# Kernel optimization log

Measured on AMD Instinct MI355X. Metric: run time of the kernel, lower is better.

Reference implementation:

```python
import jax, jax.numpy as jnp
import numpy as np

B, S, D = 2, 512, 256

def setup_inputs() -> dict:
    key = jax.random.key(0)
    k1, k2, k3, k4, k5 = jax.random.split(key, 5)
    return {
        "query": jax.random.normal(k1, (B, S, D), dtype=jnp.float32),
        "key": jax.random.normal(k2, (B, S, D), dtype=jnp.float32),
        "value": jax.random.normal(k3, (B, S, D), dtype=jnp.float32),
        "Wm_w": jax.random.normal(k4, (D, D), dtype=jnp.float32) * (1.0 / np.sqrt(D)),
        "vm_w": jax.random.normal(k5, (1, D), dtype=jnp.float32) * (1.0 / np.sqrt(D)),
    }

def reference(query, key, value, Wm_w, vm_w):
    # pairwise difference: q.unsqueeze(1) - q.unsqueeze(2) -> [B, S, S, D]
    diff = query[:, None, :, :] - query[:, :, None, :]
    # Wm (Linear, no bias): [B,S,S,D] @ Wm_w^T, then tanh
    h = jnp.tanh(jnp.einsum('bijd,ed->bije', diff, Wm_w))
    # vm (Linear D->1, no bias) + squeeze -> scores [B, S, S]
    sjt = jnp.einsum('bije,e->bij', h, vm_w[0])
    # softmax over dim=2 (eval mode: dropout is identity)
    atten = jax.nn.softmax(sjt, axis=2)
    # bmm(atten, value) -> [B, S, D]
    context = jnp.einsum('bij,bjd->bid', atten, value)
    return context, atten
```

## Files before the change

### kernel.cpp

```cpp
#include <hip/hip_runtime.h>

#define B 2
#define S 512
#define D 256
#define C2L 2.885390081777927f
#define LOG2E 1.4426950408889634f

typedef float f32x2 __attribute__((ext_vector_type(2)));
typedef unsigned int u32x2 __attribute__((ext_vector_type(2)));

__global__ __launch_bounds__(256) void proj_kernel(const float* __restrict__ q,
                                                   const float* __restrict__ W,
                                                   float* __restrict__ EJ4,
                                                   float* __restrict__ EN) {
    __shared__ float qlds[4 * D];
    const int t = threadIdx.x;
    const int b = blockIdx.x / (S / 4);
    const int i0 = (blockIdx.x % (S / 4)) * 4;
    const float* qbase = q + (size_t)(b * S + i0) * D;
    for (int idx = t; idx < 4 * D; idx += 256) qlds[idx] = qbase[idx];
    __syncthreads();
    const float* wr = W + (size_t)t * D;
    float a0 = 0.f, a1 = 0.f, a2 = 0.f, a3 = 0.f;
#pragma unroll 4
    for (int d = 0; d < D; ++d) {
        float w = wr[d];
        a0 = fmaf(qlds[d], w, a0);
        a1 = fmaf(qlds[D + d], w, a1);
        a2 = fmaf(qlds[2 * D + d], w, a2);
        a3 = fmaf(qlds[3 * D + d], w, a3);
    }
    a0 *= C2L; a1 *= C2L; a2 *= C2L; a3 *= C2L;
    float* ejb = EJ4 + (((size_t)(b * 64 + (t >> 2))) * S + i0) * 4 + (t & 3);
    ejb[0]  = __builtin_amdgcn_exp2f(a0);
    ejb[4]  = __builtin_amdgcn_exp2f(a1);
    ejb[8]  = __builtin_amdgcn_exp2f(a2);
    ejb[12] = __builtin_amdgcn_exp2f(a3);
    EN[(size_t)(b * S + i0 + 0) * D + t] = __builtin_amdgcn_exp2f(-a0);
    EN[(size_t)(b * S + i0 + 1) * D + t] = __builtin_amdgcn_exp2f(-a1);
    EN[(size_t)(b * S + i0 + 2) * D + t] = __builtin_amdgcn_exp2f(-a2);
    EN[(size_t)(b * S + i0 + 3) * D + t] = __builtin_amdgcn_exp2f(-a3);
}

__global__ __launch_bounds__(512) void fused_kernel(const float* __restrict__ EJ4,
                                                    const float* __restrict__ EN,
                                                    const float* __restrict__ vm,
                                                    const float* __restrict__ value,
                                                    float* __restrict__ att,
                                                    float* __restrict__ ctx) {
    __shared__ float en4[D][4];
    __shared__ float wl[D];
    __shared__ float a4[S][4];
    __shared__ float part[4][8][64][4];
    __shared__ float redm[4][8], reds[4][8];

    const int t = threadIdx.x;
    const int b = blockIdx.x >> 7;
    const int i0 = (blockIdx.x & 127) * 4;

    if (t < D) wl[t] = -2.f * vm[t];
    {
        const int e = t & 255, rsel = t >> 8;
        float v0 = EN[((size_t)(b * S + i0 + rsel)) * D + e];
        float v2 = EN[((size_t)(b * S + i0 + rsel + 2)) * D + e];
        en4[e][rsel * 2 + 0] = v0;
        en4[e][rsel * 2 + 1] = v2;
    }
    __syncthreads();

    f32x2 acc02 = {0.f, 0.f}, acc13 = {0.f, 0.f};
    const float4* ejp = (const float4*)EJ4 + (size_t)b * 64 * S + t;
    const f32x2 one2 = {1.f, 1.f}, two2 = {2.f, 2.f};
    const u32x2 magic = {0x7EF311C3u, 0x7EF311C3u};
#pragma unroll 4
    for (int g = 0; g < 64; ++g) {
        float4 ev4 = ejp[(size_t)g * S];
#pragma unroll
        for (int c = 0; c < 4; ++c) {
            const float ev = (c == 0) ? ev4.x : (c == 1) ? ev4.y : (c == 2) ? ev4.z : ev4.w;
            const int e = g * 4 + c;
            float4 f = *(const float4*)&en4[e][0];
            const float w = wl[e];
            f32x2 ev2 = {ev, ev};
            f32x2 f02 = {f.x, f.y}, f13 = {f.z, f.w};
            f32x2 y02 = ev2 * f02 + one2;
            f32x2 y13 = ev2 * f13 + one2;
            f32x2 r02 = {__builtin_amdgcn_rcpf(y02.x),
                         __builtin_amdgcn_rcpf(y02.y)};
            u32x2 ui = magic - __builtin_bit_cast(u32x2, y13);
            f32x2 rn = __builtin_bit_cast(f32x2, ui);
            rn = rn * (two2 - y13 * rn);
            rn = rn * (two2 - y13 * rn);
            f32x2 w2 = {w, w};
            acc02 += w2 * r02;
            acc13 += w2 * rn;
        }
    }
    float accR[4] = {acc02.x, acc13.x, acc02.y, acc13.y};

    const int lane = t & 63, wv = t >> 6;
#pragma unroll
    for (int r = 0; r < 4; ++r) {
        float lm = accR[r];
#pragma unroll
        for (int off = 32; off; off >>= 1) lm = fmaxf(lm, __shfl_xor(lm, off));
        if (lane == 0) redm[r][wv] = lm;
    }
    __syncthreads();
    float p[4];
#pragma unroll
    for (int r = 0; r < 4; ++r) {
        float m = redm[r][0];
#pragma unroll
        for (int w = 1; w < 8; ++w) m = fmaxf(m, redm[r][w]);
        p[r] = __builtin_amdgcn_exp2f((accR[r] - m) * LOG2E);
        float ls = p[r];
#pragma unroll
        for (int off = 32; off; off >>= 1) ls += __shfl_xor(ls, off);
        if (lane == 0) reds[r][wv] = ls;
    }
    __syncthreads();
#pragma unroll
    for (int r = 0; r < 4; ++r) {
        float s = 0.f;
#pragma unroll
        for (int w = 0; w < 8; ++w) s += reds[r][w];
        float a = p[r] * __builtin_amdgcn_rcpf(s);
        a4[t][r] = a;
        att[(size_t)(b * S + i0 + r) * S + t] = a;
    }
    __syncthreads();

    {
        const int dq = t & 63, js = t >> 6;
        float4 acc0 = {}, acc1 = {}, acc2 = {}, acc3 = {};
        const float* vb = value + (size_t)b * S * D + (size_t)dq * 4;
#pragma unroll 4
        for (int jj = 0; jj < 64; ++jj) {
            int j = js * 64 + jj;
            float4 v = *(const float4*)(vb + (size_t)j * D);
            float w0 = a4[j][0], w1 = a4[j][1], w2 = a4[j][2], w3 = a4[j][3];
            acc0.x = fmaf(w0, v.x, acc0.x); acc0.y = fmaf(w0, v.y, acc0.y);
            acc0.z = fmaf(w0, v.z, acc0.z); acc0.w = fmaf(w0, v.w, acc0.w);
            acc1.x = fmaf(w1, v.x, acc1.x); acc1.y = fmaf(w1, v.y, acc1.y);
            acc1.z = fmaf(w1, v.z, acc1.z); acc1.w = fmaf(w1, v.w, acc1.w);
            acc2.x = fmaf(w2, v.x, acc2.x); acc2.y = fmaf(w2, v.y, acc2.y);
            acc2.z = fmaf(w2, v.z, acc2.z); acc2.w = fmaf(w2, v.w, acc2.w);
            acc3.x = fmaf(w3, v.x, acc3.x); acc3.y = fmaf(w3, v.y, acc3.y);
            acc3.z = fmaf(w3, v.z, acc3.z); acc3.w = fmaf(w3, v.w, acc3.w);
        }
        *(float4*)&part[0][js][dq][0] = acc0;
        *(float4*)&part[1][js][dq][0] = acc1;
        *(float4*)&part[2][js][dq][0] = acc2;
        *(float4*)&part[3][js][dq][0] = acc3;
    }
    __syncthreads();
    if (t < 256) {
        const int row = t >> 6, dq = t & 63;
        float4 sum = {};
#pragma unroll
        for (int js = 0; js < 8; ++js) {
            float4 pt = *(const float4*)&part[row][js][dq][0];
            sum.x += pt.x; sum.y += pt.y; sum.z += pt.z; sum.w += pt.w;
        }
        *(float4*)(ctx + (size_t)(b * S + i0 + row) * D + (size_t)dq * 4) = sum;
    }
}

extern "C" void kernel_launch(void* const* d_in, const int* in_sizes, int n_in,
                              void* d_out, int out_size, void* d_ws, size_t ws_size,
                              hipStream_t stream) {
    const float* q = (const float*)d_in[0];
    const float* value = (const float*)d_in[2];
    const float* W = (const float*)d_in[3];
    const float* vm = (const float*)d_in[4];

    float* ctx = (float*)d_out;
    float* att = ctx + (size_t)B * S * D;
    float* EJ4 = (float*)d_ws;
    float* EN = EJ4 + (size_t)B * D * S;

    proj_kernel<<<B * (S / 4), 256, 0, stream>>>(q, W, EJ4, EN);
    fused_kernel<<<B * (S / 4), 512, 0, stream>>>(EJ4, EN, vm, value, att, ctx);
}
```

Before: 44.57 us.

## Split score reduction over E across two thread halves in fused kernel

Doubles the fused kernel's block size to 1024 threads and splits the 256-wide E reduction of the score computation into two halves of 128. Each half writes its partial sums to a new shared buffer, and the first 512 threads combine them before the softmax and context stages. The aim is more latency hiding and more waves for the transcendental-heavy score loop on a grid of only 256 blocks. The cost is extra shared memory, an additional barrier, and half the threads sitting idle during softmax and the value matmul.

```diff
diff --git a/kernel.cpp b/kernel.cpp
--- a/kernel.cpp
+++ b/kernel.cpp
@@ -42,14 +42,15 @@
     EN[(size_t)(b * S + i0 + 3) * D + t] = __builtin_amdgcn_exp2f(-a3);
 }
 
-__global__ __launch_bounds__(512) void fused_kernel(const float* __restrict__ EJ4,
-                                                    const float* __restrict__ EN,
-                                                    const float* __restrict__ vm,
-                                                    const float* __restrict__ value,
-                                                    float* __restrict__ att,
-                                                    float* __restrict__ ctx) {
+__global__ __launch_bounds__(1024) void fused_kernel(const float* __restrict__ EJ4,
+                                                     const float* __restrict__ EN,
+                                                     const float* __restrict__ vm,
+                                                     const float* __restrict__ value,
+                                                     float* __restrict__ att,
+                                                     float* __restrict__ ctx) {
     __shared__ float en4[D][4];
     __shared__ float wl[D];
+    __shared__ float4 comb[2][S];
     __shared__ float a4[S][4];
     __shared__ float part[4][8][64][4];
     __shared__ float redm[4][8], reds[4][8];
@@ -58,27 +59,26 @@
     const int b = blockIdx.x >> 7;
     const int i0 = (blockIdx.x & 127) * 4;
 
-    if (t < D) wl[t] = -2.f * vm[t];
     {
-        const int e = t & 255, rsel = t >> 8;
-        float v0 = EN[((size_t)(b * S + i0 + rsel)) * D + e];
-        float v2 = EN[((size_t)(b * S + i0 + rsel + 2)) * D + e];
-        en4[e][rsel * 2 + 0] = v0;
-        en4[e][rsel * 2 + 1] = v2;
+        const int e = t & 255, r = t >> 8;
+        const int comp = ((r & 1) << 1) | (r >> 1);
+        en4[e][comp] = EN[((size_t)(b * S + i0 + r)) * D + e];
+        if (r == 0) wl[e] = -2.f * vm[e];
     }
     __syncthreads();
 
+    const int j = t & 511, eh = t >> 9;
     f32x2 acc02 = {0.f, 0.f}, acc13 = {0.f, 0.f};
-    const float4* ejp = (const float4*)EJ4 + (size_t)b * 64 * S + t;
+    const float4* ejp = (const float4*)EJ4 + ((size_t)(b * 64 + eh * 32)) * S + j;
     const f32x2 one2 = {1.f, 1.f}, two2 = {2.f, 2.f};
     const u32x2 magic = {0x7EF311C3u, 0x7EF311C3u};
-#pragma unroll 4
-    for (int g = 0; g < 64; ++g) {
+#pragma unroll 8
+    for (int g = 0; g < 32; ++g) {
         float4 ev4 = ejp[(size_t)g * S];
 #pragma unroll
         for (int c = 0; c < 4; ++c) {
             const float ev = (c == 0) ? ev4.x : (c == 1) ? ev4.y : (c == 2) ? ev4.z : ev4.w;
-            const int e = g * 4 + c;
+            const int e = eh * 128 + g * 4 + c;
             float4 f = *(const float4*)&en4[e][0];
             const float w = wl[e];
             f32x2 ev2 = {ev, ev};
@@ -96,50 +96,60 @@
             acc13 += w2 * rn;
         }
     }
-    float accR[4] = {acc02.x, acc13.x, acc02.y, acc13.y};
+    comb[eh][j] = make_float4(acc02.x, acc13.x, acc02.y, acc13.y);
+    __syncthreads();
 
     const int lane = t & 63, wv = t >> 6;
+    float accR[4], p[4];
+    if (t < 512) {
+        float4 lo = comb[0][t], hi = comb[1][t];
+        accR[0] = lo.x + hi.x; accR[1] = lo.y + hi.y;
+        accR[2] = lo.z + hi.z; accR[3] = lo.w + hi.w;
 #pragma unroll
-    for (int r = 0; r < 4; ++r) {
-        float lm = accR[r];
+        for (int r = 0; r < 4; ++r) {
+            float lm = accR[r];
 #pragma unroll
-        for (int off = 32; off; off >>= 1) lm = fmaxf(lm, __shfl_xor(lm, off));
-        if (lane == 0) redm[r][wv] = lm;
+            for (int off = 32; off; off >>= 1) lm = fmaxf(lm, __shfl_xor(lm, off));
+            if (lane == 0) redm[r][wv] = lm;
+        }
     }
     __syncthreads();
-    float p[4];
+    if (t < 512) {
 #pragma unroll
-    for (int r = 0; r < 4; ++r) {
-        float m = redm[r][0];
+        for (int r = 0; r < 4; ++r) {
+            float m = redm[r][0];
 #pragma unroll
-        for (int w = 1; w < 8; ++w) m = fmaxf(m, redm[r][w]);
-        p[r] = __builtin_amdgcn_exp2f((accR[r] - m) * LOG2E);
-        float ls = p[r];
+            for (int w = 1; w < 8; ++w) m = fmaxf(m, redm[r][w]);
+            p[r] = __builtin_amdgcn_exp2f((accR[r] - m) * LOG2E);
+            float ls = p[r];
 #pragma unroll
-        for (int off = 32; off; off >>= 1) ls += __shfl_xor(ls, off);
-        if (lane == 0) reds[r][wv] = ls;
+            for (int off = 32; off; off >>= 1) ls += __shfl_xor(ls, off);
+            if (lane == 0) reds[r][wv] = ls;
+        }
     }
     __syncthreads();
+    if (t < 512) {
 #pragma unroll
-    for (int r = 0; r < 4; ++r) {
-        float s = 0.f;
+        for (int r = 0; r < 4; ++r) {
+            float s = 0.f;
 #pragma unroll
-        for (int w = 0; w < 8; ++w) s += reds[r][w];
-        float a = p[r] * __builtin_amdgcn_rcpf(s);
-        a4[t][r] = a;
-        att[(size_t)(b * S + i0 + r) * S + t] = a;
+            for (int w = 0; w < 8; ++w) s += reds[r][w];
+            float a = p[r] * __builtin_amdgcn_rcpf(s);
+            a4[t][r] = a;
+            att[(size_t)(b * S + i0 + r) * S + t] = a;
+        }
     }
     __syncthreads();
 
-    {
+    if (t < 512) {
         const int dq = t & 63, js = t >> 6;
         float4 acc0 = {}, acc1 = {}, acc2 = {}, acc3 = {};
         const float* vb = value + (size_t)b * S * D + (size_t)dq * 4;
 #pragma unroll 4
         for (int jj = 0; jj < 64; ++jj) {
-            int j = js * 64 + jj;
-            float4 v = *(const float4*)(vb + (size_t)j * D);
-            float w0 = a4[j][0], w1 = a4[j][1], w2 = a4[j][2], w3 = a4[j][3];
+            int jx = js * 64 + jj;
+            float4 v = *(const float4*)(vb + (size_t)jx * D);
+            float w0 = a4[jx][0], w1 = a4[jx][1], w2 = a4[jx][2], w3 = a4[jx][3];
             acc0.x = fmaf(w0, v.x, acc0.x); acc0.y = fmaf(w0, v.y, acc0.y);
             acc0.z = fmaf(w0, v.z, acc0.z); acc0.w = fmaf(w0, v.w, acc0.w);
             acc1.x = fmaf(w1, v.x, acc1.x); acc1.y = fmaf(w1, v.y, acc1.y);
@@ -181,5 +191,5 @@
     float* EN = EJ4 + (size_t)B * D * S;
 
     proj_kernel<<<B * (S / 4), 256, 0, stream>>>(q, W, EJ4, EN);
-    fused_kernel<<<B * (S / 4), 512, 0, stream>>>(EJ4, EN, vm, value, att, ctx);
+    fused_kernel<<<B * (S / 4), 1024, 0, stream>>>(EJ4, EN, vm, value, att, ctx);
 }
```

New measurement: 46.13 us. +3.5%, slower.

## Share one reciprocal per row pair and prefetch EJ4 in a register ring

Applied to the files above, without the earlier changes.

In the score loop, the two rows of each pair now share one reciprocal. It is computed on the product y0*y1 and multiplied back by the other factor, halving the rcp and Newton work per element. EJ4 loads are software-prefetched eight groups ahead into a register ring buffer, and the vm weights are merged into the same LDS array as the EN values. launch_bounds now requests two blocks per CU. The product can overflow or lose accuracy for large magnitudes, and the prefetch reads past the end of the EJ4 region on the last iteration (unused data in the workspace).

```diff
diff --git a/kernel.cpp b/kernel.cpp
--- a/kernel.cpp
+++ b/kernel.cpp
@@ -7,7 +7,6 @@
 #define LOG2E 1.4426950408889634f
 
 typedef float f32x2 __attribute__((ext_vector_type(2)));
-typedef unsigned int u32x2 __attribute__((ext_vector_type(2)));
 
 __global__ __launch_bounds__(256) void proj_kernel(const float* __restrict__ q,
                                                    const float* __restrict__ W,
@@ -42,14 +41,13 @@
     EN[(size_t)(b * S + i0 + 3) * D + t] = __builtin_amdgcn_exp2f(-a3);
 }
 
-__global__ __launch_bounds__(512) void fused_kernel(const float* __restrict__ EJ4,
-                                                    const float* __restrict__ EN,
-                                                    const float* __restrict__ vm,
-                                                    const float* __restrict__ value,
-                                                    float* __restrict__ att,
-                                                    float* __restrict__ ctx) {
-    __shared__ float en4[D][4];
-    __shared__ float wl[D];
+__global__ __launch_bounds__(512, 2) void fused_kernel(const float* __restrict__ EJ4,
+                                                       const float* __restrict__ EN,
+                                                       const float* __restrict__ vm,
+                                                       const float* __restrict__ value,
+                                                       float* __restrict__ att,
+                                                       float* __restrict__ ctx) {
+    __shared__ float enw[D][8];
     __shared__ float a4[S][4];
     __shared__ float part[4][8][64][4];
     __shared__ float redm[4][8], reds[4][8];
@@ -58,42 +56,53 @@
     const int b = blockIdx.x >> 7;
     const int i0 = (blockIdx.x & 127) * 4;
 
-    if (t < D) wl[t] = -2.f * vm[t];
     {
-        const int e = t & 255, rsel = t >> 8;
-        float v0 = EN[((size_t)(b * S + i0 + rsel)) * D + e];
-        float v2 = EN[((size_t)(b * S + i0 + rsel + 2)) * D + e];
-        en4[e][rsel * 2 + 0] = v0;
-        en4[e][rsel * 2 + 1] = v2;
+        const int e = t & 255, r = t >> 8;
+        const int row0 = i0 + 2 * r;
+        const int slot0 = r;
+        const int slot1 = 2 + r;
+        enw[e][slot0] = EN[((size_t)(b * S + row0)) * D + e];
+        enw[e][slot1] = EN[((size_t)(b * S + row0 + 1)) * D + e];
+        if (r == 0) enw[e][4] = -2.f * vm[e];
     }
     __syncthreads();
 
+    const float4* ejp = (const float4*)EJ4 + (size_t)b * 64 * S + t;
+    float4 evb[8];
+#pragma unroll
+    for (int k = 0; k < 8; ++k) evb[k] = ejp[(size_t)k * S];
+
     f32x2 acc02 = {0.f, 0.f}, acc13 = {0.f, 0.f};
-    const float4* ejp = (const float4*)EJ4 + (size_t)b * 64 * S + t;
-    const f32x2 one2 = {1.f, 1.f}, two2 = {2.f, 2.f};
-    const u32x2 magic = {0x7EF311C3u, 0x7EF311C3u};
-#pragma unroll 4
-    for (int g = 0; g < 64; ++g) {
-        float4 ev4 = ejp[(size_t)g * S];
+#pragma unroll 1
+    for (int go = 0; go < 64; go += 8) {
 #pragma unroll
-        for (int c = 0; c < 4; ++c) {
-            const float ev = (c == 0) ? ev4.x : (c == 1) ? ev4.y : (c == 2) ? ev4.z : ev4.w;
-            const int e = g * 4 + c;
-            float4 f = *(const float4*)&en4[e][0];
-            const float w = wl[e];
-            f32x2 ev2 = {ev, ev};
-            f32x2 f02 = {f.x, f.y}, f13 = {f.z, f.w};
-            f32x2 y02 = ev2 * f02 + one2;
-            f32x2 y13 = ev2 * f13 + one2;
-            f32x2 r02 = {__builtin_amdgcn_rcpf(y02.x),
-                         __builtin_amdgcn_rcpf(y02.y)};
-            u32x2 ui = magic - __builtin_bit_cast(u32x2, y13);
-            f32x2 rn = __builtin_bit_cast(f32x2, ui);
-            rn = rn * (two2 - y13 * rn);
-            rn = rn * (two2 - y13 * rn);
-            f32x2 w2 = {w, w};
-            acc02 += w2 * r02;
-            acc13 += w2 * rn;
+        for (int k = 0; k < 8; ++k) {
+            float4 ev4 = evb[k];
+            evb[k] = ejp[(size_t)(go + 8 + k) * S];
+#pragma unroll
+            for (int c = 0; c < 4; ++c) {
+                const float ev = (c == 0) ? ev4.x : (c == 1) ? ev4.y
+                               : (c == 2) ? ev4.z : ev4.w;
+                const int e = (go + k) * 4 + c;
+                float4 f = *(const float4*)&enw[e][0];
+                const float w = enw[e][4];
+                f32x2 ev2 = {ev, ev};
+                f32x2 f02 = {f.x, f.y}, f13 = {f.z, f.w};
+                f32x2 one2 = {1.f, 1.f};
+                f32x2 y02 = ev2 * f02 + one2;
+                f32x2 y13 = ev2 * f13 + one2;
+                float m02 = y02.x * y02.y;
+                float m13 = y13.x * y13.y;
+                float r02 = __builtin_amdgcn_rcpf(m02);
+                float rn = __uint_as_float(0x7EF311C3u - __float_as_uint(m13));
+                rn = rn * fmaf(-m13, rn, 2.f);
+                rn = rn * fmaf(-m13, rn, 2.f);
+                f32x2 s02 = {r02 * y02.y, r02 * y02.x};
+                f32x2 s13 = {rn * y13.y, rn * y13.x};
+                f32x2 w2 = {w, w};
+                acc02 += w2 * s02;
+                acc13 += w2 * s13;
+            }
         }
     }
     float accR[4] = {acc02.x, acc13.x, acc02.y, acc13.y};
@@ -137,9 +146,9 @@
         const float* vb = value + (size_t)b * S * D + (size_t)dq * 4;
 #pragma unroll 4
         for (int jj = 0; jj < 64; ++jj) {
-            int j = js * 64 + jj;
-            float4 v = *(const float4*)(vb + (size_t)j * D);
-            float w0 = a4[j][0], w1 = a4[j][1], w2 = a4[j][2], w3 = a4[j][3];
+            int jx = js * 64 + jj;
+            float4 v = *(const float4*)(vb + (size_t)jx * D);
+            float w0 = a4[jx][0], w1 = a4[jx][1], w2 = a4[jx][2], w3 = a4[jx][3];
             acc0.x = fmaf(w0, v.x, acc0.x); acc0.y = fmaf(w0, v.y, acc0.y);
             acc0.z = fmaf(w0, v.z, acc0.z); acc0.w = fmaf(w0, v.w, acc0.w);
             acc1.x = fmaf(w1, v.x, acc1.x); acc1.y = fmaf(w1, v.y, acc1.y);
```

New measurement: 46.25 us. 3.8% more time.
